# Optimization experiments

Measured on AMD Instinct MI355X. Metric: run time of the kernel, lower is better.

## Reference

```python
import jax, jax.numpy as jnp
import numpy as np

N = 50000
E = 500000
IN_F = 128
HEADS = 4
NEG_SLOPE = 0.2


def _gatv2_conv(x, src, dst, Wl, Wr, att, bias, concat):
    # PyG GATv2Conv (share_weights=False): x_l = lin_l(x) for source, x_r = lin_r(x) for target
    n = x.shape[0]
    H, C = att.shape
    xl = (x @ Wl.T).reshape(n, H, C)
    xr = (x @ Wr.T).reshape(n, H, C)
    # per-edge: e_ij = att . leaky_relu(xl[j] + xr[i])
    e = jax.nn.leaky_relu(xl[src] + xr[dst], negative_slope=NEG_SLOPE)  # [E,H,C]
    logit = jnp.einsum('ehc,hc->eh', e, att)  # [E,H]
    # segment softmax over destination node
    lmax = jax.ops.segment_max(logit, dst, num_segments=n)
    lmax = jnp.where(jnp.isfinite(lmax), lmax, 0.0)
    w = jnp.exp(logit - lmax[dst])
    denom = jax.ops.segment_sum(w, dst, num_segments=n)
    alpha = w / (denom[dst] + 1e-16)
    # weighted scatter-aggregate of source messages
    out = jax.ops.segment_sum(xl[src] * alpha[:, :, None], dst, num_segments=n)  # [N,H,C]
    if concat:
        return out.reshape(n, H * C) + bias
    return out.mean(axis=1) + bias


def setup_inputs() -> dict:
    key = jax.random.key(0)
    ks = jax.random.split(key, 11)
    s = 0.1
    x = jax.random.normal(ks[0], (N, IN_F), jnp.float32)
    edge_index = jax.random.randint(ks[1], (2, E), 0, N, dtype=jnp.int32)
    # layer 1: in=128 -> heads=4, C=32, concat -> out 128
    Wl1 = jax.random.normal(ks[2], (128, IN_F), jnp.float32) * s
    Wr1 = jax.random.normal(ks[3], (128, IN_F), jnp.float32) * s
    att1 = jax.random.normal(ks[4], (HEADS, 32), jnp.float32) * s
    b1 = jnp.zeros((128,), jnp.float32)
    # layer 2: in=128 -> heads=4, C=64, mean (concat=False) -> out 64
    Wl2 = jax.random.normal(ks[5], (256, 128), jnp.float32) * s
    Wr2 = jax.random.normal(ks[6], (256, 128), jnp.float32) * s
    att2 = jax.random.normal(ks[7], (HEADS, 64), jnp.float32) * s
    b2 = jnp.zeros((64,), jnp.float32)
    return {"x": x, "edge_index": edge_index, "Wl1": Wl1, "Wr1": Wr1, "att1": att1,
            "b1": b1, "Wl2": Wl2, "Wr2": Wr2, "att2": att2, "b2": b2}


def reference(x, edge_index, Wl1, Wr1, att1, b1, Wl2, Wr2, att2, b2):
    n = x.shape[0]
    loops = jnp.arange(n, dtype=edge_index.dtype)
    src = jnp.concatenate([edge_index[0], loops])  # PyG add_self_loops=True
    dst = jnp.concatenate([edge_index[1], loops])
    # dropout inactive (inference); forward body: elu between layers
    h = jax.nn.elu(_gatv2_conv(x, src, dst, Wl1, Wr1, att1, b1, concat=True))
    logits = _gatv2_conv(h, src, dst, Wl2, Wr2, att2, b2, concat=False)
    return logits
```

## Files before the change

kernel.cpp:

```cpp
#include <hip/hip_runtime.h>
#include <hip/hip_bf16.h>
#include <math.h>


typedef _Float16 half2v __attribute__((ext_vector_type(2)));
typedef _Float16 half4v __attribute__((ext_vector_type(4)));
typedef _Float16 half8v __attribute__((ext_vector_type(8)));
typedef float float4v __attribute__((ext_vector_type(4)));

template <int CTRL>
static __device__ __forceinline__ float dppadd(float x) {
  int y = __builtin_amdgcn_update_dpp(0, __float_as_int(x), CTRL, 0xf, 0xf, true);
  return x + __int_as_float(y);
}

static __device__ __forceinline__ float red8dpp(float p) {
  p = dppadd<0xB1>(p);
  p = dppadd<0x4E>(p);
  p = dppadd<0x141>(p);
  return p;
}


__global__ void fused_cvt_count_kernel(
    const float* __restrict__ x,
    const float* __restrict__ wl1, const float* __restrict__ wr1,
    const float* __restrict__ wl2, const float* __restrict__ wr2,
    _Float16* __restrict__ xb, _Float16* __restrict__ wb,
    const int* __restrict__ dst, int* __restrict__ deg, int n4x, int E) {
  int i = blockIdx.x * blockDim.x + threadIdx.x;
  int stride = gridDim.x * blockDim.x;
  int total = n4x + 24576 + E;
  for (; i < total; i += stride) {
    if (i < n4x) {
      float4 v = ((const float4*)x)[i];
      half4v o = {(_Float16)v.x, (_Float16)v.y, (_Float16)v.z, (_Float16)v.w};
      ((half4v*)xb)[i] = o;
    } else if (i < n4x + 24576) {
      int fj = (i - n4x) * 4;
      const float* src;
      int so;
      if (fj < 16384) { src = wl1; so = fj; }
      else if (fj < 32768) { src = wr1; so = fj - 16384; }
      else if (fj < 65536) { src = wl2; so = fj - 32768; }
      else { src = wr2; so = fj - 65536; }
      float4 v = *(const float4*)(src + so);
      half4v o = {(_Float16)v.x, (_Float16)v.y, (_Float16)v.z, (_Float16)v.w};
      *(half4v*)(wb + fj) = o;
    } else {
      atomicAdd(&deg[dst[i - n4x - 24576]], 1);
    }
  }
}


__global__ void partial_kernel(const int* __restrict__ deg, int* __restrict__ partial, int N) {
  int t = threadIdx.x;
  int i = blockIdx.x * 256 + t;
  int v = (i < N) ? deg[i] : 0;
  v += __shfl_xor(v, 1); v += __shfl_xor(v, 2); v += __shfl_xor(v, 4);
  v += __shfl_xor(v, 8); v += __shfl_xor(v, 16); v += __shfl_xor(v, 32);
  __shared__ int ws[4];
  if ((t & 63) == 0) ws[t >> 6] = v;
  __syncthreads();
  if (t == 0) partial[blockIdx.x] = ws[0] + ws[1] + ws[2] + ws[3];
}

__global__ void scan_final_kernel(const int* __restrict__ deg, const int* __restrict__ partial,
                                  int* __restrict__ row_ptr, int* __restrict__ cursor,
                                  int N, int E, int nb) {
  __shared__ int sp[256];
  __shared__ int s[256];
  int t = threadIdx.x;
  int pv = (t < nb) ? partial[t] : 0;
  sp[t] = pv;
  __syncthreads();
  for (int off = 1; off < 256; off <<= 1) {
    int u = (t >= off) ? sp[t - off] : 0;
    __syncthreads();
    sp[t] += u;
    __syncthreads();
  }
  int blockpre = (blockIdx.x > 0) ? sp[blockIdx.x - 1] : 0;
  int i = blockIdx.x * 256 + t;
  int v = (i < N) ? deg[i] : 0;
  s[t] = v;
  __syncthreads();
  for (int off = 1; off < 256; off <<= 1) {
    int u = (t >= off) ? s[t - off] : 0;
    __syncthreads();
    s[t] += u;
    __syncthreads();
  }
  int excl = s[t] - v + blockpre;
  if (i < N) {
    row_ptr[i] = excl;
    cursor[i] = excl;
  }
  if (blockIdx.x == 0 && t == 0) row_ptr[N] = E;
}

__global__ void fill_kernel(const int* __restrict__ src, const int* __restrict__ dst,
                            int* __restrict__ cursor, int* __restrict__ col, int E) {
  int i = blockIdx.x * blockDim.x + threadIdx.x;
  if (i < E) {
    int d = dst[i];
    int pos = atomicAdd(&cursor[d], 1);
    col[pos] = src[i];
  }
}

__global__ __launch_bounds__(256) void gemm_mfma2(
    const _Float16* __restrict__ A, const _Float16* __restrict__ Wa,
    const _Float16* __restrict__ Wb, _Float16* __restrict__ Ca,
    _Float16* __restrict__ Cb, int N, int Oa, int ldC) {
  __shared__ _Float16 lds[32768];
  int t = threadIdx.x;
  int gbase = blockIdx.y * 256;
#pragma unroll
  for (int i = 0; i < 16; ++i) {
    int c = t + i * 256;
    int row = c >> 4, kc = c & 15;
    int grow = gbase + row;
    const _Float16* srcW =
        (grow < Oa) ? (Wa + (size_t)grow * 128) : (Wb + (size_t)(grow - Oa) * 128);
    half8v v = *(const half8v*)(srcW + kc * 8);
    int off16 = (row << 4) | (kc ^ (row & 7));
    *(half8v*)((char*)lds + (off16 << 4)) = v;
  }
  __syncthreads();
  int wv = t >> 6, lane = t & 63;
  int l15 = lane & 15, l4 = lane >> 4;
  int row0 = blockIdx.x * 64 + (wv & 1) * 32;
  int colw = (wv >> 1) * 128;
  int gc = gbase + colw;
  half8v xf[2][4];
#pragma unroll
  for (int rg = 0; rg < 2; ++rg) {
    int r = row0 + rg * 16 + l15;
    bool valid = r < N;
    const half8v* Ar = (const half8v*)(A + (size_t)r * 128 + l4 * 8);
#pragma unroll
    for (int kk = 0; kk < 4; ++kk) {
      half8v z = {};
      xf[rg][kk] = valid ? Ar[kk * 4] : z;
    }
  }
  int wrow = colw + l15;
  float4v acc[2][8] = {};
#pragma unroll
  for (int kk = 0; kk < 4; ++kk) {
    int xorterm = ((kk * 4 + l4) ^ (l15 & 7)) << 4;
    const char* base = (const char*)lds + wrow * 256 + xorterm;
    half8v wf[8];
#pragma unroll
    for (int ot = 0; ot < 8; ++ot) wf[ot] = *(const half8v*)(base + ot * 4096);
#pragma unroll
    for (int ot = 0; ot < 8; ++ot) {
      acc[0][ot] = __builtin_amdgcn_mfma_f32_16x16x32_f16(wf[ot], xf[0][kk], acc[0][ot], 0, 0, 0);
      acc[1][ot] = __builtin_amdgcn_mfma_f32_16x16x32_f16(wf[ot], xf[1][kk], acc[1][ot], 0, 0, 0);
    }
  }
  bool isA = gc < Oa;
  _Float16* C = isA ? Ca : Cb;
  int cb = isA ? gc : gc - Oa;
#pragma unroll
  for (int rg = 0; rg < 2; ++rg) {
    int r = row0 + rg * 16 + l15;
    if (r < N) {
#pragma unroll
      for (int ot = 0; ot < 8; ++ot) {
        half4v o = {(_Float16)acc[rg][ot][0], (_Float16)acc[rg][ot][1],
                    (_Float16)acc[rg][ot][2], (_Float16)acc[rg][ot][3]};
        *(half4v*)(C + (size_t)r * ldC + cb + ot * 16 + l4 * 4) = o;
      }
    }
  }
}


__global__ __launch_bounds__(128) void agg1_kernel(
    const _Float16* __restrict__ xl, const _Float16* __restrict__ xr,
    const float* __restrict__ att, const float* __restrict__ bias,
    const int* __restrict__ row_ptr, const int* __restrict__ col,
    _Float16* __restrict__ hout, int N) {
  int wid = (blockIdx.x * blockDim.x + threadIdx.x) >> 6;
  int lane = threadIdx.x & 63;
  if (wid >= N) return;
  int eslot = lane >> 5, sub = lane & 31;
  const uint d0 = (uint)sub * 4u;
  const float L2E = 1.44269504f;
  half4v xrv = *(const half4v*)(xr + (((uint)wid << 7) | d0));
  float4 atf = *(const float4*)(att + d0);
  half2v atlo = {(_Float16)(atf.x * L2E), (_Float16)(atf.y * L2E)};
  half2v athi = {(_Float16)(atf.z * L2E), (_Float16)(atf.w * L2E)};
  half4v k4 = {(_Float16)0.2f, (_Float16)0.2f, (_Float16)0.2f, (_Float16)0.2f};
  int e0 = row_ptr[wid];
  int deg = row_ptr[wid + 1] - e0;
  const int* ecol = col + e0;
  float s, a0, a1, a2, a3;
  {
    half4v v = *(const half4v*)(xl + (((uint)wid << 7) | d0));
    half4v u = v + xrv;
    half4v lr = __builtin_elementwise_max(u, u * k4);
    float p = __builtin_amdgcn_fdot2((half2v){lr.x, lr.y}, atlo, 0.f, false);
    p = __builtin_amdgcn_fdot2((half2v){lr.z, lr.w}, athi, p, false);
    p = red8dpp(p);
    float w = (eslot == 0) ? exp2f(p) : 0.f;
    s = w;
    a0 = w * (float)v.x; a1 = w * (float)v.y; a2 = w * (float)v.z; a3 = w * (float)v.w;
  }
  if (deg > 0) {
    int dm1 = deg - 1;
    int cA = ecol[min(eslot, dm1)];
    int cB = ecol[min(eslot + 2, dm1)];
    int cC = ecol[min(eslot + 4, dm1)];
    half4v vA = *(const half4v*)(xl + (((uint)cA << 7) | d0));
    half4v vB = *(const half4v*)(xl + (((uint)cB << 7) | d0));
    half4v vC = *(const half4v*)(xl + (((uint)cC << 7) | d0));
    int M = deg >> 1;
    int pf = eslot + 6;
#pragma unroll 3
    for (int j = 0; j < M; ++j) {
      int cD = ecol[min(pf, dm1)];
      half4v vD = *(const half4v*)(xl + (((uint)cD << 7) | d0));
      half4v u = vA + xrv;
      half4v lr = __builtin_elementwise_max(u, u * k4);
      float p = __builtin_amdgcn_fdot2((half2v){lr.x, lr.y}, atlo, 0.f, false);
      p = __builtin_amdgcn_fdot2((half2v){lr.z, lr.w}, athi, p, false);
      p = red8dpp(p);
      float w = exp2f(p);
      s += w;
      a0 = fmaf(w, (float)vA.x, a0);
      a1 = fmaf(w, (float)vA.y, a1);
      a2 = fmaf(w, (float)vA.z, a2);
      a3 = fmaf(w, (float)vA.w, a3);
      vA = vB; vB = vC; vC = vD; pf += 2;
    }
    if (deg & 1) {
      half4v u = vA + xrv;
      half4v lr = __builtin_elementwise_max(u, u * k4);
      float p = __builtin_amdgcn_fdot2((half2v){lr.x, lr.y}, atlo, 0.f, false);
      p = __builtin_amdgcn_fdot2((half2v){lr.z, lr.w}, athi, p, false);
      p = red8dpp(p);
      float w = (eslot == 0) ? exp2f(p) : 0.f;
      s += w;
      a0 = fmaf(w, (float)vA.x, a0);
      a1 = fmaf(w, (float)vA.y, a1);
      a2 = fmaf(w, (float)vA.z, a2);
      a3 = fmaf(w, (float)vA.w, a3);
    }
  }
  s += __shfl_xor(s, 32);
  a0 += __shfl_xor(a0, 32); a1 += __shfl_xor(a1, 32);
  a2 += __shfl_xor(a2, 32); a3 += __shfl_xor(a3, 32);
  float inv = 1.f / (s + 1e-16f);
  float4 bi = *(const float4*)(bias + d0);
  float o0 = a0 * inv + bi.x, o1 = a1 * inv + bi.y;
  float o2 = a2 * inv + bi.z, o3 = a3 * inv + bi.w;
  o0 = o0 > 0.f ? o0 : __expf(o0) - 1.f;
  o1 = o1 > 0.f ? o1 : __expf(o1) - 1.f;
  o2 = o2 > 0.f ? o2 : __expf(o2) - 1.f;
  o3 = o3 > 0.f ? o3 : __expf(o3) - 1.f;
  if (eslot == 0) {
    half4v o = {(_Float16)o0, (_Float16)o1, (_Float16)o2, (_Float16)o3};
    *(half4v*)(hout + (((uint)wid << 7) | d0)) = o;
  }
}

__global__ __launch_bounds__(128) void agg2_kernel(
    const _Float16* __restrict__ xl, const _Float16* __restrict__ xr,
    const float* __restrict__ att, const float* __restrict__ bias,
    const int* __restrict__ row_ptr, const int* __restrict__ col,
    float* __restrict__ out, int N) {
  int wid = (blockIdx.x * blockDim.x + threadIdx.x) >> 6;
  int lane = threadIdx.x & 63;
  if (wid >= N) return;
  int eslot = lane >> 5, sub = lane & 31;
  const uint d0 = (uint)sub * 8u;
  const float L2E = 1.44269504f;
  const float SH = 10.f;
  half8v xrv = *(const half8v*)(xr + (((uint)wid << 8) | d0));
  float4 af0 = *(const float4*)(att + d0);
  float4 af1 = *(const float4*)(att + d0 + 4);
  half2v at[4] = {{(_Float16)(af0.x * L2E), (_Float16)(af0.y * L2E)},
                  {(_Float16)(af0.z * L2E), (_Float16)(af0.w * L2E)},
                  {(_Float16)(af1.x * L2E), (_Float16)(af1.y * L2E)},
                  {(_Float16)(af1.z * L2E), (_Float16)(af1.w * L2E)}};
  half8v k8 = {(_Float16)0.2f, (_Float16)0.2f, (_Float16)0.2f, (_Float16)0.2f,
               (_Float16)0.2f, (_Float16)0.2f, (_Float16)0.2f, (_Float16)0.2f};
  int e0 = row_ptr[wid];
  int deg = row_ptr[wid + 1] - e0;
  const int* ecol = col + e0;
  float s;
  half8v ach;
  {
    half8v v = *(const half8v*)(xl + (((uint)wid << 8) | d0));
    half8v u = v + xrv;
    half8v lr = __builtin_elementwise_max(u, u * k8);
    float p = __builtin_amdgcn_fdot2((half2v){lr[0], lr[1]}, at[0], 0.f, false);
    p = __builtin_amdgcn_fdot2((half2v){lr[2], lr[3]}, at[1], p, false);
    p = __builtin_amdgcn_fdot2((half2v){lr[4], lr[5]}, at[2], p, false);
    p = __builtin_amdgcn_fdot2((half2v){lr[6], lr[7]}, at[3], p, false);
    p = red8dpp(p);
    float w = (eslot == 0) ? exp2f(p - SH) : 0.f;
    s = w;
    _Float16 wh = (_Float16)w;
    half8v w8 = {wh, wh, wh, wh, wh, wh, wh, wh};
    ach = v * w8;
  }
  if (deg > 0) {
    int dm1 = deg - 1;
    int cA = ecol[min(eslot, dm1)];
    int cB = ecol[min(eslot + 2, dm1)];
    int cC = ecol[min(eslot + 4, dm1)];
    half8v vA = *(const half8v*)(xl + (((uint)cA << 8) | d0));
    half8v vB = *(const half8v*)(xl + (((uint)cB << 8) | d0));
    half8v vC = *(const half8v*)(xl + (((uint)cC << 8) | d0));
    int M = deg >> 1;
    int pf = eslot + 6;
#pragma unroll 3
    for (int j = 0; j < M; ++j) {
      int cD = ecol[min(pf, dm1)];
      half8v vD = *(const half8v*)(xl + (((uint)cD << 8) | d0));
      half8v u = vA + xrv;
      half8v lr = __builtin_elementwise_max(u, u * k8);
      float p = __builtin_amdgcn_fdot2((half2v){lr[0], lr[1]}, at[0], 0.f, false);
      p = __builtin_amdgcn_fdot2((half2v){lr[2], lr[3]}, at[1], p, false);
      p = __builtin_amdgcn_fdot2((half2v){lr[4], lr[5]}, at[2], p, false);
      p = __builtin_amdgcn_fdot2((half2v){lr[6], lr[7]}, at[3], p, false);
      p = red8dpp(p);
      float w = exp2f(p - SH);
      s += w;
      _Float16 wh = (_Float16)w;
      half8v w8 = {wh, wh, wh, wh, wh, wh, wh, wh};
      ach += vA * w8;
      vA = vB; vB = vC; vC = vD; pf += 2;
    }
    if (deg & 1) {
      half8v u = vA + xrv;
      half8v lr = __builtin_elementwise_max(u, u * k8);
      float p = __builtin_amdgcn_fdot2((half2v){lr[0], lr[1]}, at[0], 0.f, false);
      p = __builtin_amdgcn_fdot2((half2v){lr[2], lr[3]}, at[1], p, false);
      p = __builtin_amdgcn_fdot2((half2v){lr[4], lr[5]}, at[2], p, false);
      p = __builtin_amdgcn_fdot2((half2v){lr[6], lr[7]}, at[3], p, false);
      p = red8dpp(p);
      float w = (eslot == 0) ? exp2f(p - SH) : 0.f;
      s += w;
      _Float16 wh = (_Float16)w;
      half8v w8 = {wh, wh, wh, wh, wh, wh, wh, wh};
      ach += vA * w8;
    }
  }
  s += __shfl_xor(s, 32);
  float ac[8];
#pragma unroll
  for (int k = 0; k < 8; ++k) {
    ac[k] = (float)ach[k];
    ac[k] += __shfl_xor(ac[k], 32);
  }
  float inv = 1.f / (s + 1e-16f);
#pragma unroll
  for (int k = 0; k < 8; ++k) ac[k] *= inv;
#pragma unroll
  for (int k = 0; k < 8; ++k) {
    ac[k] += __shfl_xor(ac[k], 8);
    ac[k] += __shfl_xor(ac[k], 16);
  }
  if (lane < 8) {
    float4 b0 = *(const float4*)(bias + lane * 8);
    float4 b1v = *(const float4*)(bias + lane * 8 + 4);
    float4 o0 = make_float4(ac[0] * 0.25f + b0.x, ac[1] * 0.25f + b0.y,
                            ac[2] * 0.25f + b0.z, ac[3] * 0.25f + b0.w);
    float4 o1 = make_float4(ac[4] * 0.25f + b1v.x, ac[5] * 0.25f + b1v.y,
                            ac[6] * 0.25f + b1v.z, ac[7] * 0.25f + b1v.w);
    float* op = out + (size_t)wid * 64 + lane * 8;
    *(float4*)op = o0;
    *(float4*)(op + 4) = o1;
  }
}

extern "C" void kernel_launch(void* const* d_in, const int* in_sizes, int n_in,
                              void* d_out, int out_size, void* d_ws, size_t ws_size,
                              hipStream_t stream) {
  const float* x = (const float*)d_in[0];
  const int* ei = (const int*)d_in[1];
  const float* Wl1 = (const float*)d_in[2];
  const float* Wr1 = (const float*)d_in[3];
  const float* att1 = (const float*)d_in[4];
  const float* b1 = (const float*)d_in[5];
  const float* Wl2 = (const float*)d_in[6];
  const float* Wr2 = (const float*)d_in[7];
  const float* att2 = (const float*)d_in[8];
  const float* b2 = (const float*)d_in[9];
  float* out = (float*)d_out;

  int N = in_sizes[0] / 128;
  int E = in_sizes[1] / 2;
  const int* srcArr = ei;
  const int* dstArr = ei + E;

  char* w = (char*)d_ws;
  auto alloc = [&](size_t bytes) {
    char* p = w;
    w += (bytes + 255) & ~(size_t)255;
    return p;
  };
  int* row_ptr = (int*)alloc((size_t)(N + 1) * sizeof(int));
  int* cursor = (int*)alloc((size_t)N * sizeof(int));
  int* partial = (int*)alloc(256 * sizeof(int));
  int* col = (int*)alloc((size_t)E * sizeof(int));
  _Float16* xb = (_Float16*)alloc((size_t)N * 128 * 2);
  _Float16* wb = (_Float16*)alloc(98304 * 2);
  _Float16* hb = (_Float16*)alloc((size_t)N * 128 * 2);
  _Float16* xl1 = (_Float16*)alloc((size_t)N * 128 * 2);
  _Float16* xr1 = (_Float16*)alloc((size_t)N * 128 * 2);
  _Float16* xl2 = (_Float16*)alloc((size_t)N * 256 * 2);
  _Float16* xr2 = (_Float16*)alloc((size_t)N * 256 * 2);

  const _Float16* wl1b = wb;
  const _Float16* wr1b = wb + 16384;
  const _Float16* wl2b = wb + 32768;
  const _Float16* wr2b = wb + 65536;

  hipMemsetAsync(cursor, 0, (size_t)N * sizeof(int), stream);
  fused_cvt_count_kernel<<<2048, 256, 0, stream>>>(x, Wl1, Wr1, Wl2, Wr2, xb, wb,
                                                   dstArr, cursor, N * 32, E);

  int nb = (N + 255) / 256;
  partial_kernel<<<nb, 256, 0, stream>>>(cursor, partial, N);
  scan_final_kernel<<<nb, 256, 0, stream>>>(cursor, partial, row_ptr, cursor, N, E, nb);
  fill_kernel<<<(E + 255) / 256, 256, 0, stream>>>(srcArr, dstArr, cursor, col, E);

  int gx = (N + 63) / 64;
  int aggBlocks = (N * 64 + 127) / 128;
  gemm_mfma2<<<dim3(gx, 1), 256, 0, stream>>>(xb, wl1b, wr1b, xl1, xr1, N, 128, 128);
  agg1_kernel<<<aggBlocks, 128, 0, stream>>>(xl1, xr1, att1, b1, row_ptr, col, hb, N);

  gemm_mfma2<<<dim3(gx, 2), 256, 0, stream>>>(hb, wl2b, wr2b, xl2, xr2, N, 256, 256);
  agg2_kernel<<<aggBlocks, 128, 0, stream>>>(xl2, xr2, att2, b2, row_ptr, col, out, N);
}
```

Baseline: 190.9 us.

## Fuse x fp32-to-fp16 conversion into GEMM and widen agg1 to 4 edges per wave

Drops the separate x to fp16 conversion pass and its fp16 buffer. The layer-1 GEMM now loads fp32 x directly and converts it in registers, which removes one full write and re-read of x. The layer-1 aggregation is restructured so each wave handles 4 edges at a time with 16 lanes per edge and 8 features per lane, instead of 2 edges with 32 lanes and 4 features. This means wider loads, more edge parallelism and a shorter dot-product reduction, at the cost of more registers and extra cross-lane shuffles at the end.

```diff
diff --git a/kernel.cpp b/kernel.cpp
--- a/kernel.cpp
+++ b/kernel.cpp
@@ -12,6 +12,12 @@
 static __device__ __forceinline__ float dppadd(float x) {
   int y = __builtin_amdgcn_update_dpp(0, __float_as_int(x), CTRL, 0xf, 0xf, true);
   return x + __int_as_float(y);
+}
+
+static __device__ __forceinline__ float red4dpp(float p) {
+  p = dppadd<0xB1>(p);
+  p = dppadd<0x4E>(p);
+  return p;
 }
 
 static __device__ __forceinline__ float red8dpp(float p) {
@@ -22,22 +28,17 @@
 }
 
 
-__global__ void fused_cvt_count_kernel(
-    const float* __restrict__ x,
+__global__ void cvt_w_count_kernel(
     const float* __restrict__ wl1, const float* __restrict__ wr1,
     const float* __restrict__ wl2, const float* __restrict__ wr2,
-    _Float16* __restrict__ xb, _Float16* __restrict__ wb,
-    const int* __restrict__ dst, int* __restrict__ deg, int n4x, int E) {
+    _Float16* __restrict__ wb,
+    const int* __restrict__ dst, int* __restrict__ deg, int E) {
   int i = blockIdx.x * blockDim.x + threadIdx.x;
   int stride = gridDim.x * blockDim.x;
-  int total = n4x + 24576 + E;
+  int total = 24576 + E;
   for (; i < total; i += stride) {
-    if (i < n4x) {
-      float4 v = ((const float4*)x)[i];
-      half4v o = {(_Float16)v.x, (_Float16)v.y, (_Float16)v.z, (_Float16)v.w};
-      ((half4v*)xb)[i] = o;
-    } else if (i < n4x + 24576) {
-      int fj = (i - n4x) * 4;
+    if (i < 24576) {
+      int fj = i * 4;
       const float* src;
       int so;
       if (fj < 16384) { src = wl1; so = fj; }
@@ -48,7 +49,7 @@
       half4v o = {(_Float16)v.x, (_Float16)v.y, (_Float16)v.z, (_Float16)v.w};
       *(half4v*)(wb + fj) = o;
     } else {
-      atomicAdd(&deg[dst[i - n4x - 24576]], 1);
+      atomicAdd(&deg[dst[i - 24576]], 1);
     }
   }
 }
@@ -110,8 +111,9 @@
   }
 }
 
+template <bool AF32>
 __global__ __launch_bounds__(256) void gemm_mfma2(
-    const _Float16* __restrict__ A, const _Float16* __restrict__ Wa,
+    const void* __restrict__ Av, const _Float16* __restrict__ Wa,
     const _Float16* __restrict__ Wb, _Float16* __restrict__ Ca,
     _Float16* __restrict__ Cb, int N, int Oa, int ldC) {
   __shared__ _Float16 lds[32768];
@@ -139,11 +141,26 @@
   for (int rg = 0; rg < 2; ++rg) {
     int r = row0 + rg * 16 + l15;
     bool valid = r < N;
-    const half8v* Ar = (const half8v*)(A + (size_t)r * 128 + l4 * 8);
-#pragma unroll
-    for (int kk = 0; kk < 4; ++kk) {
-      half8v z = {};
-      xf[rg][kk] = valid ? Ar[kk * 4] : z;
+    if constexpr (AF32) {
+      const float* Ar = (const float*)Av + (size_t)r * 128 + l4 * 8;
+#pragma unroll
+      for (int kk = 0; kk < 4; ++kk) {
+        half8v z = {};
+        if (valid) {
+          float4 q0 = *(const float4*)(Ar + kk * 32);
+          float4 q1 = *(const float4*)(Ar + kk * 32 + 4);
+          z = half8v{(_Float16)q0.x, (_Float16)q0.y, (_Float16)q0.z, (_Float16)q0.w,
+                     (_Float16)q1.x, (_Float16)q1.y, (_Float16)q1.z, (_Float16)q1.w};
+        }
+        xf[rg][kk] = z;
+      }
+    } else {
+      const half8v* Ar = (const half8v*)((const _Float16*)Av + (size_t)r * 128 + l4 * 8);
+#pragma unroll
+      for (int kk = 0; kk < 4; ++kk) {
+        half8v z = {};
+        xf[rg][kk] = valid ? Ar[kk * 4] : z;
+      }
     }
   }
   int wrow = colw + l15;
@@ -187,84 +204,71 @@
   int wid = (blockIdx.x * blockDim.x + threadIdx.x) >> 6;
   int lane = threadIdx.x & 63;
   if (wid >= N) return;
-  int eslot = lane >> 5, sub = lane & 31;
-  const uint d0 = (uint)sub * 4u;
+  int eslot = lane >> 4, sub = lane & 15;
+  const uint d0 = (uint)sub * 8u;
   const float L2E = 1.44269504f;
-  half4v xrv = *(const half4v*)(xr + (((uint)wid << 7) | d0));
-  float4 atf = *(const float4*)(att + d0);
-  half2v atlo = {(_Float16)(atf.x * L2E), (_Float16)(atf.y * L2E)};
-  half2v athi = {(_Float16)(atf.z * L2E), (_Float16)(atf.w * L2E)};
-  half4v k4 = {(_Float16)0.2f, (_Float16)0.2f, (_Float16)0.2f, (_Float16)0.2f};
+  half8v xrv = *(const half8v*)(xr + (((uint)wid << 7) | d0));
+  float4 af0 = *(const float4*)(att + d0);
+  float4 af1 = *(const float4*)(att + d0 + 4);
+  half2v at4[4] = {{(_Float16)(af0.x * L2E), (_Float16)(af0.y * L2E)},
+                   {(_Float16)(af0.z * L2E), (_Float16)(af0.w * L2E)},
+                   {(_Float16)(af1.x * L2E), (_Float16)(af1.y * L2E)},
+                   {(_Float16)(af1.z * L2E), (_Float16)(af1.w * L2E)}};
+  half8v k8 = {(_Float16)0.2f, (_Float16)0.2f, (_Float16)0.2f, (_Float16)0.2f,
+               (_Float16)0.2f, (_Float16)0.2f, (_Float16)0.2f, (_Float16)0.2f};
   int e0 = row_ptr[wid];
   int deg = row_ptr[wid + 1] - e0;
   const int* ecol = col + e0;
-  float s, a0, a1, a2, a3;
-  {
-    half4v v = *(const half4v*)(xl + (((uint)wid << 7) | d0));
-    half4v u = v + xrv;
-    half4v lr = __builtin_elementwise_max(u, u * k4);
-    float p = __builtin_amdgcn_fdot2((half2v){lr.x, lr.y}, atlo, 0.f, false);
-    p = __builtin_amdgcn_fdot2((half2v){lr.z, lr.w}, athi, p, false);
-    p = red8dpp(p);
-    float w = (eslot == 0) ? exp2f(p) : 0.f;
-    s = w;
-    a0 = w * (float)v.x; a1 = w * (float)v.y; a2 = w * (float)v.z; a3 = w * (float)v.w;
-  }
+  float s = 0.f, a[8] = {};
+  auto edge = [&](half8v v, bool valid) {
+    half8v u = v + xrv;
+    half8v lr = __builtin_elementwise_max(u, u * k8);
+    float pA = __builtin_amdgcn_fdot2((half2v){lr[0], lr[1]}, at4[0], 0.f, false);
+    pA = __builtin_amdgcn_fdot2((half2v){lr[2], lr[3]}, at4[1], pA, false);
+    float pB = __builtin_amdgcn_fdot2((half2v){lr[4], lr[5]}, at4[2], 0.f, false);
+    pB = __builtin_amdgcn_fdot2((half2v){lr[6], lr[7]}, at4[3], pB, false);
+    float p = red4dpp(pA + pB);
+    float w = valid ? exp2f(p) : 0.f;
+    s += w;
+#pragma unroll
+    for (int k = 0; k < 8; ++k) a[k] = fmaf(w, (float)v[k], a[k]);
+  };
+  auto ld = [&](uint node) { return *(const half8v*)(xl + ((node << 7) | d0)); };
+  edge(ld((uint)wid), eslot == 0);
   if (deg > 0) {
     int dm1 = deg - 1;
-    int cA = ecol[min(eslot, dm1)];
-    int cB = ecol[min(eslot + 2, dm1)];
-    int cC = ecol[min(eslot + 4, dm1)];
-    half4v vA = *(const half4v*)(xl + (((uint)cA << 7) | d0));
-    half4v vB = *(const half4v*)(xl + (((uint)cB << 7) | d0));
-    half4v vC = *(const half4v*)(xl + (((uint)cC << 7) | d0));
-    int M = deg >> 1;
-    int pf = eslot + 6;
-#pragma unroll 3
+    half8v vA = ld((uint)ecol[min(eslot, dm1)]);
+    half8v vB = ld((uint)ecol[min(eslot + 4, dm1)]);
+    half8v vC = ld((uint)ecol[min(eslot + 8, dm1)]);
+    int M = deg >> 2, pf = eslot + 12;
+#pragma unroll 2
     for (int j = 0; j < M; ++j) {
-      int cD = ecol[min(pf, dm1)];
-      half4v vD = *(const half4v*)(xl + (((uint)cD << 7) | d0));
-      half4v u = vA + xrv;
-      half4v lr = __builtin_elementwise_max(u, u * k4);
-      float p = __builtin_amdgcn_fdot2((half2v){lr.x, lr.y}, atlo, 0.f, false);
-      p = __builtin_amdgcn_fdot2((half2v){lr.z, lr.w}, athi, p, false);
-      p = red8dpp(p);
-      float w = exp2f(p);
-      s += w;
-      a0 = fmaf(w, (float)vA.x, a0);
-      a1 = fmaf(w, (float)vA.y, a1);
-      a2 = fmaf(w, (float)vA.z, a2);
-      a3 = fmaf(w, (float)vA.w, a3);
-      vA = vB; vB = vC; vC = vD; pf += 2;
-    }
-    if (deg & 1) {
-      half4v u = vA + xrv;
-      half4v lr = __builtin_elementwise_max(u, u * k4);
-      float p = __builtin_amdgcn_fdot2((half2v){lr.x, lr.y}, atlo, 0.f, false);
-      p = __builtin_amdgcn_fdot2((half2v){lr.z, lr.w}, athi, p, false);
-      p = red8dpp(p);
-      float w = (eslot == 0) ? exp2f(p) : 0.f;
-      s += w;
-      a0 = fmaf(w, (float)vA.x, a0);
-      a1 = fmaf(w, (float)vA.y, a1);
-      a2 = fmaf(w, (float)vA.z, a2);
-      a3 = fmaf(w, (float)vA.w, a3);
-    }
-  }
-  s += __shfl_xor(s, 32);
-  a0 += __shfl_xor(a0, 32); a1 += __shfl_xor(a1, 32);
-  a2 += __shfl_xor(a2, 32); a3 += __shfl_xor(a3, 32);
+      half8v vD = ld((uint)ecol[min(pf, dm1)]);
+      edge(vA, true);
+      vA = vB; vB = vC; vC = vD; pf += 4;
+    }
+    int T = deg & 3;
+    if (T) edge(vA, eslot < T);
+  }
+  s += __shfl_xor(s, 16); s += __shfl_xor(s, 32);
+#pragma unroll
+  for (int k = 0; k < 8; ++k) {
+    a[k] += __shfl_xor(a[k], 16);
+    a[k] += __shfl_xor(a[k], 32);
+  }
   float inv = 1.f / (s + 1e-16f);
-  float4 bi = *(const float4*)(bias + d0);
-  float o0 = a0 * inv + bi.x, o1 = a1 * inv + bi.y;
-  float o2 = a2 * inv + bi.z, o3 = a3 * inv + bi.w;
-  o0 = o0 > 0.f ? o0 : __expf(o0) - 1.f;
-  o1 = o1 > 0.f ? o1 : __expf(o1) - 1.f;
-  o2 = o2 > 0.f ? o2 : __expf(o2) - 1.f;
-  o3 = o3 > 0.f ? o3 : __expf(o3) - 1.f;
   if (eslot == 0) {
-    half4v o = {(_Float16)o0, (_Float16)o1, (_Float16)o2, (_Float16)o3};
-    *(half4v*)(hout + (((uint)wid << 7) | d0)) = o;
+    float4 b0 = *(const float4*)(bias + d0);
+    float4 b1 = *(const float4*)(bias + d0 + 4);
+    float bb[8] = {b0.x, b0.y, b0.z, b0.w, b1.x, b1.y, b1.z, b1.w};
+    half8v o;
+#pragma unroll
+    for (int k = 0; k < 8; ++k) {
+      float tv = a[k] * inv + bb[k];
+      tv = tv > 0.f ? tv : __expf(tv) - 1.f;
+      o[k] = (_Float16)tv;
+    }
+    *(half8v*)(hout + (((uint)wid << 7) | d0)) = o;
   }
 }
 
@@ -410,7 +414,6 @@
   int* cursor = (int*)alloc((size_t)N * sizeof(int));
   int* partial = (int*)alloc(256 * sizeof(int));
   int* col = (int*)alloc((size_t)E * sizeof(int));
-  _Float16* xb = (_Float16*)alloc((size_t)N * 128 * 2);
   _Float16* wb = (_Float16*)alloc(98304 * 2);
   _Float16* hb = (_Float16*)alloc((size_t)N * 128 * 2);
   _Float16* xl1 = (_Float16*)alloc((size_t)N * 128 * 2);
@@ -424,8 +427,7 @@
   const _Float16* wr2b = wb + 65536;
 
   hipMemsetAsync(cursor, 0, (size_t)N * sizeof(int), stream);
-  fused_cvt_count_kernel<<<2048, 256, 0, stream>>>(x, Wl1, Wr1, Wl2, Wr2, xb, wb,
-                                                   dstArr, cursor, N * 32, E);
+  cvt_w_count_kernel<<<1024, 256, 0, stream>>>(Wl1, Wr1, Wl2, Wr2, wb, dstArr, cursor, E);
 
   int nb = (N + 255) / 256;
   partial_kernel<<<nb, 256, 0, stream>>>(cursor, partial, N);
@@ -434,9 +436,9 @@
 
   int gx = (N + 63) / 64;
   int aggBlocks = (N * 64 + 127) / 128;
-  gemm_mfma2<<<dim3(gx, 1), 256, 0, stream>>>(xb, wl1b, wr1b, xl1, xr1, N, 128, 128);
+  gemm_mfma2<true><<<dim3(gx, 1), 256, 0, stream>>>(x, wl1b, wr1b, xl1, xr1, N, 128, 128);
   agg1_kernel<<<aggBlocks, 128, 0, stream>>>(xl1, xr1, att1, b1, row_ptr, col, hb, N);
 
-  gemm_mfma2<<<dim3(gx, 2), 256, 0, stream>>>(hb, wl2b, wr2b, xl2, xr2, N, 256, 256);
+  gemm_mfma2<false><<<dim3(gx, 2), 256, 0, stream>>>(hb, wl2b, wr2b, xl2, xr2, N, 256, 256);
   agg2_kernel<<<aggBlocks, 128, 0, stream>>>(xl2, xr2, att2, b2, row_ptr, col, out, N);
 }
```

After: 186.6 us. 1.02x faster.
